# Optimization experiments

Hardware: AMD Instinct MI355X
Metric: run time of the kernel (lower is better)

## Reference

```python
import jax, jax.numpy as jnp
import numpy as np

B, T, D_MODEL, D_HEAD = 4, 4096, 512, 64  # batch, token_depth, token_len, d_head
D_K = 64
NEG = -1.0e9  # mask fill value used by the torch module


def setup_inputs() -> dict:
    key = jax.random.key(0)
    kx, kq, kk, kv = jax.random.split(key, 4)
    x = jax.random.normal(kx, (B, T, D_MODEL), dtype=jnp.float32)
    # nn.Linear(token_len, d_head, bias=False) -> weight shape [d_head, token_len]
    Wq = jax.random.normal(kq, (D_HEAD, D_MODEL), dtype=jnp.float32) * 0.02
    Wk = jax.random.normal(kk, (D_HEAD, D_MODEL), dtype=jnp.float32) * 0.02
    Wv = jax.random.normal(kv, (D_HEAD, D_MODEL), dtype=jnp.float32) * 0.02
    return {"x": x, "Wq": Wq, "Wk": Wk, "Wv": Wv}


def reference(x, Wq, Wk, Wv):
    # q/k/v projections: y = x @ W.T  (Linear with bias=False)
    q = jnp.einsum("btd,hd->bth", x, Wq)  # [B,T,D_HEAD]
    k = jnp.einsum("btd,hd->bth", x, Wk)
    v = jnp.einsum("btd,hd->bth", x, Wv)

    scores = jnp.einsum("bth,bsh->bts", q, k)  # [B,T,T]

    # additive causal mask: upper triangle (diagonal=1) filled with -1e9
    t_idx = jnp.arange(T)
    mask = jnp.where(t_idx[None, :] > t_idx[:, None], NEG, 0.0).astype(scores.dtype)
    scores = scores + mask[None, :, :]

    sqrt_dk = jnp.sqrt(jnp.asarray(D_K, dtype=scores.dtype))
    # NOTE: original code applies softmax over dim=1 (the query axis), not -1.
    attn = jax.nn.softmax(scores / sqrt_dk, axis=1)
    out = jnp.einsum("bts,bsh->bth", attn, v)  # [B,T,D_HEAD]
    return out
```

## Files before the change

### kernel.cpp

```cpp
#include <hip/hip_runtime.h>

#define B_ 4
#define T_ 4096
#define DM 512
#define DH 64
#define CS 512
#define CTS 1024

typedef short short8 __attribute__((ext_vector_type(8)));
typedef short bf16x4 __attribute__((ext_vector_type(4)));
typedef float f32x4 __attribute__((ext_vector_type(4)));
typedef float float8 __attribute__((ext_vector_type(8)));

__device__ inline short f2bf(float f) {
    unsigned u = __float_as_uint(f);
    u += 0x7fffu + ((u >> 16) & 1u);
    return (short)(u >> 16);
}
__device__ inline float bf2f(short s) {
    return __uint_as_float(((unsigned)(unsigned short)s) << 16);
}
__device__ inline short8 cvt8(const float* p) {
    float8 v = *(const float8*)p;
    short8 r;
#pragma unroll
    for (int j = 0; j < 8; j++) r[j] = f2bf(v[j]);
    return r;
}
__device__ inline unsigned cvt_pk_bf16(float a, float b) {
    unsigned r;
    asm("v_cvt_pk_bf16_f32 %0, %1, %2" : "=v"(r) : "v"(a), "v"(b));
    return r;
}
__device__ inline bf16x4 pmask4(f32x4 d, int sbase, int t) {
    float p[4];
#pragma unroll
    for (int r = 0; r < 4; r++) {
        float e = __expf(d[r] * 0.125f);
        p[r] = (sbase + r <= t) ? e : 0.f;
    }
    union { unsigned u[2]; bf16x4 v; } z;
    z.u[0] = cvt_pk_bf16(p[0], p[1]);
    z.u[1] = cvt_pk_bf16(p[2], p[3]);
    return z.v;
}

__global__ __launch_bounds__(256) void k_wcvt(
    const float* __restrict__ Wq, const float* __restrict__ Wk,
    const float* __restrict__ Wv, short* __restrict__ wb)
{
    int e = (blockIdx.x * 256 + threadIdx.x) * 8;
    int m = e / (DH * DM);
    int off = e - m * (DH * DM);
    const float* W = (m == 0) ? Wq : (m == 1) ? Wk : Wv;
    *(short8*)(wb + e) = cvt8(W + off);
}

__global__ __launch_bounds__(256) void k_proj(
    const float* __restrict__ x, const short* __restrict__ wb,
    short* __restrict__ qb, short* __restrict__ kb, short* __restrict__ vb)
{
    int tid = threadIdx.x;
    int lane = tid & 63, w = tid >> 6;
    int l16 = lane & 15, quad = lane >> 4;
    int r = blockIdx.x;
    int b = r >> 6, tile = r & 63;
    int t0w = tile * 64 + w * 16;
    long base_x = ((long)(b * T_ + t0w + l16)) * DM;

    f32x4 acc[3][4];
#pragma unroll
    for (int m = 0; m < 3; m++)
#pragma unroll
        for (int i = 0; i < 4; i++) acc[m][i] = (f32x4)(0.f);

    for (int kc = 0; kc < DM; kc += 32) {
        short8 af = cvt8(x + base_x + kc + quad * 8);
#pragma unroll
        for (int m = 0; m < 3; m++)
#pragma unroll
            for (int h4 = 0; h4 < 4; h4++) {
                short8 bf = *(const short8*)(wb + (long)m * DH * DM +
                                             (long)(h4 * 16 + l16) * DM + kc + quad * 8);
                acc[m][h4] = __builtin_amdgcn_mfma_f32_16x16x32_bf16(af, bf, acc[m][h4], 0, 0, 0);
            }
    }
#pragma unroll
    for (int m = 0; m < 3; m++) {
        short* outp = (m == 0) ? qb : (m == 1) ? kb : vb;
#pragma unroll
        for (int h4 = 0; h4 < 4; h4++)
#pragma unroll
            for (int r4 = 0; r4 < 4; r4++) {
                int t = t0w + quad * 4 + r4;
                outp[((long)(b * T_ + t)) * DH + h4 * 16 + l16] = f2bf(acc[m][h4][r4]);
            }
    }
}

__global__ __launch_bounds__(256, 4) void k_stats(
    const short* __restrict__ qb, const short* __restrict__ kb, float* __restrict__ lsum)
{
    __shared__ short Qb[128 * 72];
    int tid = threadIdx.x;
    int lane = tid & 63, w = tid >> 6;
    int l16 = lane & 15, quad = lane >> 4;
    const int NC = T_ / CTS;
    int chunk = blockIdx.x % NC;
    int st = (blockIdx.x / NC) & 31;
    int b = blockIdx.x / (NC * 32);
    int c0 = chunk * CTS, cend = c0 + CTS;
    int s0blk = st * 128;
    if (cend <= s0blk) return;
    int s0w = s0blk + w * 32;
    long bq = (long)b * T_ * DH;

    const short8* kp0 = (const short8*)(kb + bq + (long)(s0w + l16) * DH + quad * 8);
    short8 a00 = kp0[0], a01 = kp0[4];
    const short8* kp1 = (const short8*)(kb + bq + (long)(s0w + 16 + l16) * DH + quad * 8);
    short8 a10 = kp1[0], a11 = kp1[4];

    int t_lo = (c0 > s0blk) ? c0 : s0blk;
    int nsteps = (cend - t_lo) >> 7;
    float acc0[4] = {0.f, 0.f, 0.f, 0.f};
    float acc1[4] = {0.f, 0.f, 0.f, 0.f};

    for (int stp = 0; stp < nsteps; stp++) {
        int t0 = t_lo + stp * 128;
#pragma unroll
        for (int p = 0; p < 4; p++) {
            int idx = p * 256 + tid;
            int row = idx >> 3, col = idx & 7;
            *(short8*)(Qb + row * 72 + col * 8) =
                *(const short8*)(qb + bq + (long)(t0 + row) * DH + col * 8);
        }
        __syncthreads();
        for (int sub = 0; sub < 8; sub++) {
            int tt = t0 + sub * 16;
            if (tt + 15 >= s0w) {
                short8 b0 = *(const short8*)(Qb + (sub * 16 + l16) * 72 + quad * 8);
                short8 b1 = *(const short8*)(Qb + (sub * 16 + l16) * 72 + 32 + quad * 8);
                int t = tt + l16;
                f32x4 d0 = (f32x4)(0.f);
                d0 = __builtin_amdgcn_mfma_f32_16x16x32_bf16(a00, b0, d0, 0, 0, 0);
                d0 = __builtin_amdgcn_mfma_f32_16x16x32_bf16(a01, b1, d0, 0, 0, 0);
#pragma unroll
                for (int r = 0; r < 4; r++) {
                    int s = s0w + quad * 4 + r;
                    float p = __expf(d0[r] * 0.125f);
                    acc0[r] += (t >= s) ? p : 0.f;
                }
                if (tt + 15 >= s0w + 16) {
                    f32x4 d1 = (f32x4)(0.f);
                    d1 = __builtin_amdgcn_mfma_f32_16x16x32_bf16(a10, b0, d1, 0, 0, 0);
                    d1 = __builtin_amdgcn_mfma_f32_16x16x32_bf16(a11, b1, d1, 0, 0, 0);
#pragma unroll
                    for (int r = 0; r < 4; r++) {
                        int s = s0w + 16 + quad * 4 + r;
                        float p = __expf(d1[r] * 0.125f);
                        acc1[r] += (t >= s) ? p : 0.f;
                    }
                }
            }
        }
        __syncthreads();
    }
#pragma unroll
    for (int r = 0; r < 4; r++) {
        float v = acc0[r];
        v += __shfl_xor(v, 1, 16); v += __shfl_xor(v, 2, 16);
        v += __shfl_xor(v, 4, 16); v += __shfl_xor(v, 8, 16);
        if (l16 == 0) atomicAdd(&lsum[b * T_ + s0w + quad * 4 + r], v);
        float v1 = acc1[r];
        v1 += __shfl_xor(v1, 1, 16); v1 += __shfl_xor(v1, 2, 16);
        v1 += __shfl_xor(v1, 4, 16); v1 += __shfl_xor(v1, 8, 16);
        if (l16 == 0) atomicAdd(&lsum[b * T_ + s0w + 16 + quad * 4 + r], v1);
    }
}

__global__ __launch_bounds__(256) void k_vt(
    const short* __restrict__ vb, const float* __restrict__ lsum, short* __restrict__ vTc)
{
    int tid = threadIdx.x;
    int b = blockIdx.x >> 6;
    int s0 = (blockIdx.x & 63) * 64;
    int h = tid & 63, g = tid >> 6;
    long vbase = ((long)(b * T_) + s0 + g * 16) * DH + h;
    long lbase = (long)b * T_ + s0 + g * 16;
    short8 lo, hi;
#pragma unroll
    for (int k2 = 0; k2 < 8; k2++) {
        float rl = 1.0f / lsum[lbase + k2];
        lo[k2] = f2bf(bf2f(vb[vbase + (long)k2 * DH]) * rl);
        float rh = 1.0f / lsum[lbase + 8 + k2];
        hi[k2] = f2bf(bf2f(vb[vbase + (long)(8 + k2) * DH]) * rh);
    }
    long ob = ((long)(b * 256 + (s0 >> 4) + g) * 64 + h) * 16;
    *(short8*)(vTc + ob) = lo;
    *(short8*)(vTc + ob + 8) = hi;
}

__global__ __launch_bounds__(256, 4) void k_out(
    const short* __restrict__ qb, const short* __restrict__ kb,
    const short* __restrict__ vTc, float* __restrict__ out)
{
    __shared__ short Kb[128 * 72];
    __shared__ short Vb[8 * 64 * 20];
    int tid = threadIdx.x;
    int lane = tid & 63, w = tid >> 6;
    int l16 = lane & 15, quad = lane >> 4;
    const int NC = T_ / CS;
    int chunk = blockIdx.x % NC;
    int strip = (blockIdx.x / NC) & 31;
    int b = blockIdx.x / (NC * 32);
    int c0 = chunk * CS;
    int blk_tmax = strip * 128 + 127;
    if (c0 > blk_tmax) return;
    int s_hi = (c0 + CS < blk_tmax + 1) ? c0 + CS : blk_tmax + 1;
    int nsteps = (s_hi - c0 + 127) >> 7;
    int t0w = strip * 128 + w * 32;
    long bq = (long)b * T_ * DH;

    const short8* qp0 = (const short8*)(qb + bq + (long)(t0w + l16) * DH + quad * 8);
    short8 q00 = qp0[0], q01 = qp0[4];
    const short8* qp1 = (const short8*)(qb + bq + (long)(t0w + 16 + l16) * DH + quad * 8);
    short8 q10 = qp1[0], q11 = qp1[4];
    const short* vTb = vTc + (long)b * (T_ / 16) * DH * 16;

    f32x4 o0[4], o1[4];
#pragma unroll
    for (int i = 0; i < 4; i++) { o0[i] = (f32x4)(0.f); o1[i] = (f32x4)(0.f); }
    int t0 = t0w + l16, t1 = t0 + 16;

    for (int stp = 0; stp < nsteps; stp++) {
        int s0 = c0 + stp * 128;
#pragma unroll
        for (int p = 0; p < 4; p++) {
            int idx = p * 256 + tid;
            int row = idx >> 3, col = idx & 7;
            *(short8*)(Kb + row * 72 + col * 8) =
                *(const short8*)(kb + bq + (long)(s0 + row) * DH + col * 8);
        }
        int g0 = s0 >> 4;
#pragma unroll
        for (int p = 0; p < 4; p++) {
            int idx = p * 256 + tid;
            int g = idx >> 7, rem = idx & 127;
            int h = rem >> 1, c = rem & 1;
            const short* src = vTb + (long)(g0 + g) * 1024 + h * 16 + c * 8;
            short* dst = Vb + g * 1280 + h * 20 + c * 8;
            *(bf16x4*)(dst) = *(const bf16x4*)(src);
            *(bf16x4*)(dst + 4) = *(const bf16x4*)(src + 4);
        }
        __syncthreads();

        for (int sub = 0; sub < 8; sub++) {
            int sc = s0 + sub * 16;
            if (sc > t0w + 31) break;
            short8 a0 = *(const short8*)(Kb + (sub * 16 + l16) * 72 + quad * 8);
            short8 a1 = *(const short8*)(Kb + (sub * 16 + l16) * 72 + 32 + quad * 8);

            f32x4 d1 = (f32x4)(0.f);
            d1 = __builtin_amdgcn_mfma_f32_16x16x32_bf16(a0, q10, d1, 0, 0, 0);
            d1 = __builtin_amdgcn_mfma_f32_16x16x32_bf16(a1, q11, d1, 0, 0, 0);
            bf16x4 pa1 = pmask4(d1, sc + quad * 4, t1);

            bf16x4 pa0 = (bf16x4)(short)0;
            if (sc <= t0w + 15) {
                f32x4 d0 = (f32x4)(0.f);
                d0 = __builtin_amdgcn_mfma_f32_16x16x32_bf16(a0, q00, d0, 0, 0, 0);
                d0 = __builtin_amdgcn_mfma_f32_16x16x32_bf16(a1, q01, d0, 0, 0, 0);
                pa0 = pmask4(d0, sc + quad * 4, t0);
            }
            const short* vc = Vb + sub * 1280 + quad * 4;
#pragma unroll
            for (int h4 = 0; h4 < 4; h4++) {
                bf16x4 bv = *(const bf16x4*)(vc + (h4 * 16 + l16) * 20);
                o1[h4] = __builtin_amdgcn_mfma_f32_16x16x16bf16_1k(pa1, bv, o1[h4], 0, 0, 0);
                o0[h4] = __builtin_amdgcn_mfma_f32_16x16x16bf16_1k(pa0, bv, o0[h4], 0, 0, 0);
            }
        }
        __syncthreads();
    }
#pragma unroll
    for (int h4 = 0; h4 < 4; h4++)
#pragma unroll
        for (int r = 0; r < 4; r++) {
            int t = t0w + quad * 4 + r;
            atomicAdd(&out[bq + (long)t * DH + h4 * 16 + l16], o0[h4][r]);
            atomicAdd(&out[bq + (long)(t + 16) * DH + h4 * 16 + l16], o1[h4][r]);
        }
}

extern "C" void kernel_launch(void* const* d_in, const int* in_sizes, int n_in,
                              void* d_out, int out_size, void* d_ws, size_t ws_size,
                              hipStream_t stream) {
    const float* x  = (const float*)d_in[0];
    const float* Wq = (const float*)d_in[1];
    const float* Wk = (const float*)d_in[2];
    const float* Wv = (const float*)d_in[3];
    float* out = (float*)d_out;

    char* ws = (char*)d_ws;
    short* qb   = (short*)(ws);
    short* kb   = (short*)(ws + (2l << 20));
    short* vb   = (short*)(ws + (4l << 20));
    short* vTc  = (short*)(ws + (6l << 20));
    short* wb   = (short*)(ws + (8l << 20));
    float* lsum = (float*)(ws + (9l << 20));

    hipMemsetAsync(out, 0, (size_t)out_size * sizeof(float), stream);
    hipMemsetAsync(lsum, 0, (size_t)(B_ * T_) * sizeof(float), stream);

    k_wcvt<<<dim3(48), dim3(256), 0, stream>>>(Wq, Wk, Wv, wb);
    k_proj<<<dim3(B_ * T_ / 64), dim3(256), 0, stream>>>(x, wb, qb, kb, vb);
    k_stats<<<dim3(B_ * 32 * (T_ / CTS)), dim3(256), 0, stream>>>(qb, kb, lsum);
    k_vt<<<dim3(B_ * T_ / 64), dim3(256), 0, stream>>>(vb, lsum, vTc);
    k_out<<<dim3(B_ * 32 * (T_ / CS)), dim3(256), 0, stream>>>(qb, kb, vTc, out);
}
```

Baseline: 164.7 us.

## Stage X and weight tiles through LDS in QKV projection kernel

The projection kernel now cooperatively loads 64-wide K slices of x (converted to bf16) and all three weight matrices into padded shared-memory tiles, then runs the MFMAs from LDS. Previously every wave re-read the weight fragments from global memory and loaded x directly. This cuts redundant global and L2 traffic for the weights and coalesces the loads. In exchange it adds two block barriers per K step and LDS pressure, and the launch bounds now request four blocks per CU.

```diff
diff --git a/kernel.cpp b/kernel.cpp
--- a/kernel.cpp
+++ b/kernel.cpp
@@ -56,34 +56,49 @@
     *(short8*)(wb + e) = cvt8(W + off);
 }
 
-__global__ __launch_bounds__(256) void k_proj(
+__global__ __launch_bounds__(256, 4) void k_proj(
     const float* __restrict__ x, const short* __restrict__ wb,
     short* __restrict__ qb, short* __restrict__ kb, short* __restrict__ vb)
 {
+    __shared__ short Xs[64 * 72];
+    __shared__ short Ws[192 * 72];
     int tid = threadIdx.x;
     int lane = tid & 63, w = tid >> 6;
     int l16 = lane & 15, quad = lane >> 4;
-    int r = blockIdx.x;
-    int b = r >> 6, tile = r & 63;
-    int t0w = tile * 64 + w * 16;
-    long base_x = ((long)(b * T_ + t0w + l16)) * DM;
-
-    f32x4 acc[3][4];
-#pragma unroll
-    for (int m = 0; m < 3; m++)
-#pragma unroll
-        for (int i = 0; i < 4; i++) acc[m][i] = (f32x4)(0.f);
-
-    for (int kc = 0; kc < DM; kc += 32) {
-        short8 af = cvt8(x + base_x + kc + quad * 8);
-#pragma unroll
-        for (int m = 0; m < 3; m++)
-#pragma unroll
-            for (int h4 = 0; h4 < 4; h4++) {
-                short8 bf = *(const short8*)(wb + (long)m * DH * DM +
-                                             (long)(h4 * 16 + l16) * DM + kc + quad * 8);
-                acc[m][h4] = __builtin_amdgcn_mfma_f32_16x16x32_bf16(af, bf, acc[m][h4], 0, 0, 0);
-            }
+    int b = blockIdx.x >> 6;
+    int tile = blockIdx.x & 63;
+    int t0 = tile * 64;
+    long xbase = ((long)(b * T_ + t0)) * DM;
+
+    f32x4 acc[12];
+#pragma unroll
+    for (int i = 0; i < 12; i++) acc[i] = (f32x4)(0.f);
+
+    for (int kc = 0; kc < DM; kc += 64) {
+#pragma unroll
+        for (int p = 0; p < 2; p++) {
+            int idx = p * 256 + tid;
+            int row = idx >> 3, col = (idx & 7) * 8;
+            *(short8*)(Xs + row * 72 + col) = cvt8(x + xbase + (long)row * DM + kc + col);
+        }
+#pragma unroll
+        for (int p = 0; p < 6; p++) {
+            int idx = p * 256 + tid;
+            int row = idx >> 3, col = (idx & 7) * 8;
+            *(short8*)(Ws + row * 72 + col) =
+                *(const short8*)(wb + (long)row * DM + kc + col);
+        }
+        __syncthreads();
+#pragma unroll
+        for (int ks = 0; ks < 2; ks++) {
+            short8 af = *(const short8*)(Xs + (w * 16 + l16) * 72 + ks * 32 + quad * 8);
+#pragma unroll
+            for (int hh = 0; hh < 12; hh++) {
+                short8 bf = *(const short8*)(Ws + (hh * 16 + l16) * 72 + ks * 32 + quad * 8);
+                acc[hh] = __builtin_amdgcn_mfma_f32_16x16x32_bf16(af, bf, acc[hh], 0, 0, 0);
+            }
+        }
+        __syncthreads();
     }
 #pragma unroll
     for (int m = 0; m < 3; m++) {
@@ -92,8 +107,8 @@
         for (int h4 = 0; h4 < 4; h4++)
 #pragma unroll
             for (int r4 = 0; r4 < 4; r4++) {
-                int t = t0w + quad * 4 + r4;
-                outp[((long)(b * T_ + t)) * DH + h4 * 16 + l16] = f2bf(acc[m][h4][r4]);
+                int t = t0 + w * 16 + quad * 4 + r4;
+                outp[((long)(b * T_ + t)) * DH + h4 * 16 + l16] = f2bf(acc[m * 4 + h4][r4]);
             }
     }
 }
```

New measurement: 166.7 us. Within noise of the previous version (+1.2%).
